# Performance work log

Hardware: AMD Instinct MI355X
Metric: run time of the kernel (lower is better)

Reference implementation:

```python
import jax, jax.numpy as jnp
import numpy as np

# SLAYER neuron / simulation parameters (from network.yaml)
THETA = 10.0      # spike threshold
TAU_SR = 10.0     # SRM (psp) kernel time constant
TAU_REF = 1.0     # refractory kernel time constant
SCALE_REF = 2.0   # refractory scale (kernel = -scaleRef*theta*alpha(t))
TS = 1.0          # simulation step (ms)
TK = 100          # FIR truncation length for the psp kernel (tauSr=10 -> fully decayed)

B, NIN, NHID, NOUT, T = 32, 2312, 512, 10, 350

# discrete refractory kernel ref[n] = C_REF * n * D_REF**n  (alpha shape)
D_REF = float(np.exp(-TS / TAU_REF))
C_REF = float(-SCALE_REF * THETA * np.e * TS / TAU_REF)


def srm_kernel():
    # eps(t) = (t/tauSr) * exp(1 - t/tauSr), peak value 1 at t = tauSr
    t = jnp.arange(TK, dtype=jnp.float32) * TS
    return (t / TAU_SR) * jnp.exp(1.0 - t / TAU_SR)


def psp(x):
    """Causal FIR filter along time. x: [B, C, T] -> [B, C, T]."""
    b, c, t = x.shape
    k = srm_kernel()[::-1].reshape(1, 1, TK)  # lax.conv correlates, so flip
    xp = jnp.pad(x.reshape(b * c, 1, t), ((0, 0), (0, 0), (TK - 1, 0)))
    y = jax.lax.conv_general_dilated(xp, k, (1,), 'VALID')
    return y.reshape(b, c, t)


def dense(W, x):
    # 1x1 conv over channels, applied at every time step
    return jnp.einsum('oi,bit->bot', W, x)


@jax.custom_vjp
def spike_fn(u):
    return (u >= THETA).astype(u.dtype)

def _spike_fwd(u):
    return spike_fn(u), u

def _spike_bwd(u, g):
    # SLAYER surrogate gradient: rho(u) = scaleRho * exp(-|u - theta| / tauRho)
    return (g * jnp.exp(-jnp.abs(u - THETA) / 1.0),)

spike_fn.defvjp(_spike_fwd, _spike_bwd)


def spike_layer(u_in):
    """Threshold-and-refractory spike dynamics via a 2-state IIR realization of
    the alpha refractory kernel. u_in: [B, C, T] -> spikes [B, C, T]."""
    uT = jnp.moveaxis(u_in, -1, 0)  # [T, B, C]
    zero = jnp.zeros(uT.shape[1:], uT.dtype)

    def step(carry, u_t):
        a, b = carry  # a = conv(spikes, D^n), b = conv(spikes, n*D^n)
        u = u_t + C_REF * b          # membrane = psp drive + refractory
        s = spike_fn(u)
        a_new = D_REF * a + s
        b_new = D_REF * b + D_REF * a
        return (a_new, b_new), s

    _, sT = jax.lax.scan(step, (zero, zero), uT)
    return jnp.moveaxis(sT, 0, -1)


def setup_inputs() -> dict:
    key = jax.random.key(0)
    k1, k2, k3 = jax.random.split(key, 3)
    spikeInput = (jax.random.uniform(k1, (B, NIN, T)) < 0.05).astype(jnp.float32)
    W1 = jax.random.normal(k2, (NHID, NIN), dtype=jnp.float32) * 0.05
    W2 = jax.random.normal(k3, (NOUT, NHID), dtype=jnp.float32) * 0.05
    return {"spikeInput": spikeInput, "W1": W1, "W2": W2}


def reference(spikeInput, W1, W2):
    s1 = spike_layer(dense(W1, psp(spikeInput)))
    s2 = spike_layer(dense(W2, psp(s1)))
    return s2
```

## Files before the change

### kernel.cpp

```cpp
#include <hip/hip_runtime.h>
#include <stdint.h>

#define B_SZ   32
#define NIN    2312
#define NHID   512
#define NOUT   10
#define T_SZ   350
#define NW32   73
#define NW64   8
#define NHALF  256
#define NROW   2313

#define DS_D   0.9048374180359595
#define CS_D   0.2718281828459045
#define D100_D 4.5399929762484854e-05
#define DREF_F 0.36787944117144233f
#define CREF_F -54.36563656918091f

#define NCHUNK 7
#define CLEN   50
#define NPF    10

__global__ __launch_bounds__(384) void k12(const float* __restrict__ x,
                                           const float* __restrict__ W1,
                                           uint32_t* __restrict__ bits1,
                                           float* __restrict__ W1s) {
    __shared__ float lds[32 * T_SZ];
    const int bid = blockIdx.x;
    const int tid = threadIdx.x;
    if (bid < NW32 * B_SZ) {
        const int w = bid % NW32;
        const int b = bid / NW32;
        const int rows = (NIN - (w << 5) < 32) ? (NIN - (w << 5)) : 32;
        const float* base = x + ((size_t)(b * NIN + (w << 5))) * T_SZ;
        const int nf4 = (rows * T_SZ) >> 2;
        for (int f = tid; f < nf4; f += 384)
            ((float4*)lds)[f] = ((const float4*)base)[f];
        __syncthreads();
        if (tid < T_SZ) {
            uint32_t bits = 0;
            for (int j = 0; j < rows; ++j)
                bits |= (lds[j * T_SZ + tid] > 0.5f) ? (1u << j) : 0u;
            bits1[(size_t)(b * T_SZ + tid) * NW32 + w] = bits;
        }
    } else if (bid < NW32 * B_SZ + NW32 * 16) {
        float (*tile)[33] = (float (*)[33])lds;
        const int bb = bid - NW32 * B_SZ;
        const int i0 = (bb % NW32) * 32, o0 = (bb / NW32) * 32;
        const int tx = tid & 31, ty = tid >> 5;
#pragma unroll
        for (int r = 0; r < 3; ++r) {
            int row = ty + 12 * r;
            if (row < 32) {
                int o = o0 + row, i = i0 + tx;
                if (i < NIN) tile[row][tx] = W1[(size_t)o * NIN + i];
            }
        }
        __syncthreads();
#pragma unroll
        for (int r = 0; r < 3; ++r) {
            int row = ty + 12 * r;
            if (row < 32) {
                int i = i0 + row, o = o0 + tx;
                if (i < NIN)
                    W1s[((size_t)(o >> 8) * NROW + i) * NHALF + (o & 255)] = tile[tx][row];
            }
        }
    } else {
        if (tid < NHALF) {
            W1s[((size_t)0 * NROW + NIN) * NHALF + tid] = 0.0f;
            W1s[((size_t)1 * NROW + NIN) * NHALF + tid] = 0.0f;
        }
    }
}

__global__ __launch_bounds__(256) void k3_dense1(const uint32_t* __restrict__ bits1,
                                                 const float* __restrict__ W1s,
                                                 float* __restrict__ z1ct) {
    __shared__ uint32_t words[128];
    __shared__ uint16_t pfx[80];
    __shared__ uint16_t idxbuf[NIN + 16];
    __shared__ float red[3][NHALF];
    __shared__ float fin[NHALF];

    const int id = blockIdx.x;
    const int h = (id >> 2) & 1;
    const int bt = ((id >> 3) << 2) | (id & 3);
    const int tid = threadIdx.x;
    const int wv = tid >> 6, lane = tid & 63;

    if (tid < 128) words[tid] = (tid < NW32) ? bits1[(size_t)bt * NW32 + tid] : 0u;
    __syncthreads();

    if (wv == 0) {
        uint32_t w0 = words[lane];
        uint32_t w1 = words[lane + 64];
        int p0 = __popc(w0), p1 = __popc(w1);
        int s0 = p0, s1 = p1;
#pragma unroll
        for (int off = 1; off < 64; off <<= 1) {
            int u0 = __shfl_up(s0, off);
            int u1 = __shfl_up(s1, off);
            if (lane >= off) { s0 += u0; s1 += u1; }
        }
        int tot0 = __shfl(s0, 63);
        pfx[lane] = (uint16_t)(s0 - p0);
        if (lane < 9) pfx[lane + 64] = (uint16_t)(tot0 + s1 - p1);
        if (lane == 8) pfx[73] = (uint16_t)(tot0 + s1);
    }
    __syncthreads();

    const int ntot = pfx[73];
    const int npad = (ntot + 15) & ~15;
    if (tid < NW32) {
        uint32_t m = words[tid];
        int p = pfx[tid];
        while (m) {
            int j = __builtin_ctz(m);
            m &= m - 1;
            idxbuf[p++] = (uint16_t)((tid << 5) + j);
        }
    }
    if (tid >= 240) {
        int k = tid - 240;
        if (ntot + k < npad) idxbuf[ntot + k] = (uint16_t)NIN;
    }
    __syncthreads();

    const float* Wh = W1s + (size_t)h * NROW * NHALF;
    float4 acc = make_float4(0.f, 0.f, 0.f, 0.f);
    for (int r = wv; r < npad; r += 16) {
        int i0 = idxbuf[r], i1 = idxbuf[r + 4], i2 = idxbuf[r + 8], i3 = idxbuf[r + 12];
        float4 v0 = ((const float4*)(Wh + (size_t)i0 * NHALF))[lane];
        float4 v1 = ((const float4*)(Wh + (size_t)i1 * NHALF))[lane];
        float4 v2 = ((const float4*)(Wh + (size_t)i2 * NHALF))[lane];
        float4 v3 = ((const float4*)(Wh + (size_t)i3 * NHALF))[lane];
        acc.x += v0.x; acc.y += v0.y; acc.z += v0.z; acc.w += v0.w;
        acc.x += v1.x; acc.y += v1.y; acc.z += v1.z; acc.w += v1.w;
        acc.x += v2.x; acc.y += v2.y; acc.z += v2.z; acc.w += v2.w;
        acc.x += v3.x; acc.y += v3.y; acc.z += v3.z; acc.w += v3.w;
    }
    if (wv > 0) ((float4*)red[wv - 1])[lane] = acc;
    __syncthreads();
    if (wv == 0) {
        float4 a1 = ((float4*)red[0])[lane];
        float4 a2 = ((float4*)red[1])[lane];
        float4 a3 = ((float4*)red[2])[lane];
        acc.x = ((acc.x + a1.x) + a2.x) + a3.x;
        acc.y = ((acc.y + a1.y) + a2.y) + a3.y;
        acc.z = ((acc.z + a1.z) + a2.z) + a3.z;
        acc.w = ((acc.w + a1.w) + a2.w) + a3.w;
        ((float4*)fin)[lane] = acc;
    }
    __syncthreads();
    const int och = (h << 8) + tid;
    const int oc = och >> 6, l6 = och & 63;
    const int b = bt / T_SZ, t = bt - b * T_SZ;
    z1ct[((size_t)(b * NW64 + oc) * T_SZ + t) * 64 + l6] = fin[tid];
}

__global__ __launch_bounds__(512) void k45(const float* __restrict__ z1ct,
                                           const float* __restrict__ W2,
                                           float* __restrict__ z2ct) {
    __shared__ float W2s[NHID * NOUT];
    __shared__ uint64_t sw[CLEN][NW64];
    const int tid = threadIdx.x;
    const int wv = tid >> 6, lane = tid & 63;
    const int b = blockIdx.x / NCHUNK;
    const int ck = blockIdx.x % NCHUNK;
    const int tstart = ck * CLEN;
    const int tend = tstart + CLEN;
    const int t0 = (tstart >= 100) ? tstart - 100 : 0;

    for (int k = tid; k < NHID * NOUT; k += 512) {
        int c = k / NOUT, o = k - c * NOUT;
        W2s[k] = W2[(size_t)o * NHID + c];
    }

    const float* base = z1ct + (size_t)(b * NW64 + wv) * T_SZ * 64 + lane;
    double A = 0.0, Bs = 0.0, A2 = 0.0, Bs2 = 0.0;
    float ra = 0.0f, rb = 0.0f;
    const double TAIL = D100_D * CS_D;
    float xb[NPF], xdb[NPF];
#pragma unroll
    for (int i = 0; i < NPF; ++i) {
        int t = t0 + i;
        xb[i] = base[(size_t)t * 64];
        int td = t - 100;
        xdb[i] = (td >= 0) ? base[(size_t)td * 64] : 0.0f;
    }
    for (int tb = t0; tb < tend; tb += NPF) {
#pragma unroll
        for (int i = 0; i < NPF; ++i) {
            const int t = tb + i;
            float x = xb[i], xd = xdb[i];
            const int tn = t + NPF;
            xb[i] = (tn < T_SZ) ? base[(size_t)tn * 64] : 0.0f;
            const int td = tn - 100;
            xdb[i] = (td >= 0) ? base[(size_t)td * 64] : 0.0f;
            Bs = DS_D * Bs + DS_D * A;
            A = DS_D * A + (double)x;
            Bs2 = DS_D * Bs2 + DS_D * A2;
            A2 = DS_D * A2 + (double)xd;
            double y = CS_D * Bs - TAIL * (Bs2 + 100.0 * A2);
            float u = (float)y + CREF_F * rb;
            float s = (u >= 10.0f) ? 1.0f : 0.0f;
            float ran = DREF_F * ra + s;
            float rbn = DREF_F * rb + DREF_F * ra;
            ra = ran; rb = rbn;
            uint64_t mball = __ballot(s != 0.0f);
            if (t >= tstart && lane == 0) sw[t - tstart][wv] = mball;
        }
    }
    __syncthreads();

    if (tid < CLEN * NOUT) {
        const int tr = tid / NOUT;
        const int o = tid - tr * NOUT;
        const int t = tstart + tr;
        float acc = 0.f;
#pragma unroll
        for (int w2 = 0; w2 < NW64; ++w2) {
            uint64_t m = sw[tr][w2];
            while (m) {
                int j = __builtin_ctzll(m);
                m &= m - 1;
                acc += W2s[((w2 << 6) + j) * NOUT + o];
            }
        }
        const int bo = b * NOUT + o;
        z2ct[((size_t)(bo >> 6) * T_SZ + t) * 64 + (bo & 63)] = acc;
    }
}

__global__ __launch_bounds__(64) void k6_fir_scan2(const float* __restrict__ z2ct,
                                                   float* __restrict__ out) {
    const int lane = threadIdx.x;
    const int g = blockIdx.x / NCHUNK;
    const int ck = blockIdx.x % NCHUNK;
    const int tstart = ck * CLEN;
    const int tend = tstart + CLEN;
    const int t0 = (tstart >= 100) ? tstart - 100 : 0;
    const int bo = (g << 6) + lane;
    const float* base = z2ct + (size_t)g * T_SZ * 64 + lane;
    float* op = out + (size_t)bo * T_SZ;
    double A = 0.0, Bs = 0.0, A2 = 0.0, Bs2 = 0.0;
    float ra = 0.0f, rb = 0.0f;
    const double TAIL = D100_D * CS_D;
    float xb[NPF], xdb[NPF];
#pragma unroll
    for (int i = 0; i < NPF; ++i) {
        int t = t0 + i;
        xb[i] = base[(size_t)t * 64];
        int td = t - 100;
        xdb[i] = (td >= 0) ? base[(size_t)td * 64] : 0.0f;
    }
    for (int tb = t0; tb < tend; tb += NPF) {
#pragma unroll
        for (int i = 0; i < NPF; ++i) {
            const int t = tb + i;
            float x = xb[i], xd = xdb[i];
            const int tn = t + NPF;
            xb[i] = (tn < T_SZ) ? base[(size_t)tn * 64] : 0.0f;
            const int td = tn - 100;
            xdb[i] = (td >= 0) ? base[(size_t)td * 64] : 0.0f;
            Bs = DS_D * Bs + DS_D * A;
            A = DS_D * A + (double)x;
            Bs2 = DS_D * Bs2 + DS_D * A2;
            A2 = DS_D * A2 + (double)xd;
            double y = CS_D * Bs - TAIL * (Bs2 + 100.0 * A2);
            float u = (float)y + CREF_F * rb;
            float s = (u >= 10.0f) ? 1.0f : 0.0f;
            float ran = DREF_F * ra + s;
            float rbn = DREF_F * rb + DREF_F * ra;
            ra = ran; rb = rbn;
            if (t >= tstart) op[t] = s;
        }
    }
}

extern "C" void kernel_launch(void* const* d_in, const int* in_sizes, int n_in,
                              void* d_out, int out_size, void* d_ws, size_t ws_size,
                              hipStream_t stream) {
    const float* spikeInput = (const float*)d_in[0];
    const float* W1 = (const float*)d_in[1];
    const float* W2 = (const float*)d_in[2];
    float* out = (float*)d_out;

    char* ws = (char*)d_ws;
    float* W1s = (float*)(ws + 0);
    uint32_t* bits1 = (uint32_t*)(ws + 4737024);
    float* z1ct = (float*)(ws + 8007424);
    float* z2ct = (float*)(ws + 4737024);

    k12<<<NW32 * B_SZ + NW32 * 16 + 1, 384, 0, stream>>>(spikeInput, W1, bits1, W1s);
    k3_dense1<<<B_SZ * T_SZ * 2, 256, 0, stream>>>(bits1, W1s, z1ct);
    k45<<<B_SZ * NCHUNK, 512, 0, stream>>>(z1ct, W2, z2ct);
    k6_fir_scan2<<<5 * NCHUNK, 64, 0, stream>>>(z2ct, out);
}
```

Measured before the change: 315.8 us.

## Initialize PSP IIR state directly via 4-way strided decomposition instead of long burn-in

In the second-layer kernel, chunks other than the first no longer replay up to 100 steps of the serial IIR recurrence before their window. Each chunk now seeds the A/Bs state (and the delayed-tail A2/Bs2 state) with four interleaved sub-recurrences using D^4, combined in closed form. The burn-in before the window is cut to 40 steps. This shortens the sequential dependency chain per chunk, at the cost of extra loads and double-precision math up front and a possible change in the spike dynamics' warm-up behaviour.

```diff
diff --git a/kernel.cpp b/kernel.cpp
--- a/kernel.cpp
+++ b/kernel.cpp
@@ -12,6 +12,9 @@
 #define NROW   2313
 
 #define DS_D   0.9048374180359595
+#define DS2_D  0.8187307530779818
+#define DS3_D  0.7408182206817179
+#define DS4_D  0.6703200460356393
 #define CS_D   0.2718281828459045
 #define D100_D 4.5399929762484854e-05
 #define DREF_F 0.36787944117144233f
@@ -19,6 +22,7 @@
 
 #define NCHUNK 7
 #define CLEN   50
+#define BURN   40
 #define NPF    10
 
 __global__ __launch_bounds__(384) void k12(const float* __restrict__ x,
@@ -170,7 +174,7 @@
     const int ck = blockIdx.x % NCHUNK;
     const int tstart = ck * CLEN;
     const int tend = tstart + CLEN;
-    const int t0 = (tstart >= 100) ? tstart - 100 : 0;
+    const int t0 = (ck == 0) ? 0 : tstart - BURN;
 
     for (int k = tid; k < NHID * NOUT; k += 512) {
         int c = k / NOUT, o = k - c * NOUT;
@@ -181,6 +185,43 @@
     double A = 0.0, Bs = 0.0, A2 = 0.0, Bs2 = 0.0;
     float ra = 0.0f, rb = 0.0f;
     const double TAIL = D100_D * CS_D;
+
+    if (ck != 0) {
+        const int hi1 = t0 - 1;
+        const int hi2 = t0 - 101;
+        double F0=0,F1=0,F2=0,F3=0, G0=0,G1=0,G2=0,G3=0;
+        double P0=0,P1=0,P2=0,P3=0, Q0=0,Q1=0,Q2=0,Q3=0;
+#pragma unroll
+        for (int q = 0; q < 25; ++q) {
+            const int ta3 = hi1 - 99 + 4 * q;
+            float x3 = 0.f, x2 = 0.f, x1 = 0.f, x0 = 0.f;
+            if (ta3     >= 0) x3 = base[(size_t)(ta3    ) * 64];
+            if (ta3 + 1 >= 0) x2 = base[(size_t)(ta3 + 1) * 64];
+            if (ta3 + 2 >= 0) x1 = base[(size_t)(ta3 + 2) * 64];
+            if (ta3 + 3 >= 0) x0 = base[(size_t)(ta3 + 3) * 64];
+            G3 = DS4_D * G3 + DS4_D * F3; F3 = DS4_D * F3 + (double)x3;
+            G2 = DS4_D * G2 + DS4_D * F2; F2 = DS4_D * F2 + (double)x2;
+            G1 = DS4_D * G1 + DS4_D * F1; F1 = DS4_D * F1 + (double)x1;
+            G0 = DS4_D * G0 + DS4_D * F0; F0 = DS4_D * F0 + (double)x0;
+            const int tb3 = hi2 - 99 + 4 * q;
+            float y3 = 0.f, y2 = 0.f, y1 = 0.f, y0 = 0.f;
+            if (tb3     >= 0) y3 = base[(size_t)(tb3    ) * 64];
+            if (tb3 + 1 >= 0) y2 = base[(size_t)(tb3 + 1) * 64];
+            if (tb3 + 2 >= 0) y1 = base[(size_t)(tb3 + 2) * 64];
+            if (tb3 + 3 >= 0) y0 = base[(size_t)(tb3 + 3) * 64];
+            Q3 = DS4_D * Q3 + DS4_D * P3; P3 = DS4_D * P3 + (double)y3;
+            Q2 = DS4_D * Q2 + DS4_D * P2; P2 = DS4_D * P2 + (double)y2;
+            Q1 = DS4_D * Q1 + DS4_D * P1; P1 = DS4_D * P1 + (double)y1;
+            Q0 = DS4_D * Q0 + DS4_D * P0; P0 = DS4_D * P0 + (double)y0;
+        }
+        A   = F0 + DS_D * F1 + DS2_D * F2 + DS3_D * F3;
+        Bs  = 4.0 * G0 + DS_D * (F1 + 4.0 * G1)
+            + DS2_D * (2.0 * F2 + 4.0 * G2) + DS3_D * (3.0 * F3 + 4.0 * G3);
+        A2  = P0 + DS_D * P1 + DS2_D * P2 + DS3_D * P3;
+        Bs2 = 4.0 * Q0 + DS_D * (P1 + 4.0 * Q1)
+            + DS2_D * (2.0 * P2 + 4.0 * Q2) + DS3_D * (3.0 * P3 + 4.0 * Q3);
+    }
+
     float xb[NPF], xdb[NPF];
 #pragma unroll
     for (int i = 0; i < NPF; ++i) {
```

After: 376.7 us. +19.3%, slower.

## Split fused scan+dense2 kernel into full-length scan and separate dense2

Applied to the files above, without the earlier changes.

The fused k45 kernel, which recomputed a 100-step warmup window of the first-layer FIR/refractory scan for each of seven time chunks, is split in two. A new scan kernel runs each 64-channel group once over the whole time axis and writes spike ballots to workspace, and a separate dense2 kernel reads those ballots per chunk. This removes the redundant warmup recomputation, but the scan becomes one long serial pass per wave across only 256 single-wave blocks. It also adds an extra launch and a global round trip for the ballots.

```diff
diff --git a/kernel.cpp b/kernel.cpp
--- a/kernel.cpp
+++ b/kernel.cpp
@@ -20,6 +20,7 @@
 #define NCHUNK 7
 #define CLEN   50
 #define NPF    10
+#define SNPF   14
 
 __global__ __launch_bounds__(384) void k12(const float* __restrict__ x,
                                            const float* __restrict__ W1,
@@ -159,42 +160,29 @@
     z1ct[((size_t)(b * NW64 + oc) * T_SZ + t) * 64 + l6] = fin[tid];
 }
 
-__global__ __launch_bounds__(512) void k45(const float* __restrict__ z1ct,
-                                           const float* __restrict__ W2,
-                                           float* __restrict__ z2ct) {
-    __shared__ float W2s[NHID * NOUT];
-    __shared__ uint64_t sw[CLEN][NW64];
-    const int tid = threadIdx.x;
-    const int wv = tid >> 6, lane = tid & 63;
-    const int b = blockIdx.x / NCHUNK;
-    const int ck = blockIdx.x % NCHUNK;
-    const int tstart = ck * CLEN;
-    const int tend = tstart + CLEN;
-    const int t0 = (tstart >= 100) ? tstart - 100 : 0;
-
-    for (int k = tid; k < NHID * NOUT; k += 512) {
-        int c = k / NOUT, o = k - c * NOUT;
-        W2s[k] = W2[(size_t)o * NHID + c];
-    }
-
-    const float* base = z1ct + (size_t)(b * NW64 + wv) * T_SZ * 64 + lane;
+__global__ __launch_bounds__(64) void k4_scan1(const float* __restrict__ z1ct,
+                                               uint64_t* __restrict__ ballots) {
+    const int lane = threadIdx.x;
+    const int bg = blockIdx.x;
+    const float* base = z1ct + (size_t)bg * T_SZ * 64 + lane;
+    const int b = bg >> 3, g = bg & 7;
+    uint64_t* bout = ballots + (size_t)b * T_SZ * NW64 + g;
+
     double A = 0.0, Bs = 0.0, A2 = 0.0, Bs2 = 0.0;
     float ra = 0.0f, rb = 0.0f;
     const double TAIL = D100_D * CS_D;
-    float xb[NPF], xdb[NPF];
-#pragma unroll
-    for (int i = 0; i < NPF; ++i) {
-        int t = t0 + i;
-        xb[i] = base[(size_t)t * 64];
-        int td = t - 100;
-        xdb[i] = (td >= 0) ? base[(size_t)td * 64] : 0.0f;
-    }
-    for (int tb = t0; tb < tend; tb += NPF) {
-#pragma unroll
-        for (int i = 0; i < NPF; ++i) {
+    float xb[SNPF], xdb[SNPF];
+#pragma unroll
+    for (int i = 0; i < SNPF; ++i) {
+        xb[i] = base[(size_t)i * 64];
+        xdb[i] = 0.0f;
+    }
+    for (int tb = 0; tb < T_SZ; tb += SNPF) {
+#pragma unroll
+        for (int i = 0; i < SNPF; ++i) {
             const int t = tb + i;
             float x = xb[i], xd = xdb[i];
-            const int tn = t + NPF;
+            const int tn = t + SNPF;
             xb[i] = (tn < T_SZ) ? base[(size_t)tn * 64] : 0.0f;
             const int td = tn - 100;
             xdb[i] = (td >= 0) ? base[(size_t)td * 64] : 0.0f;
@@ -209,8 +197,28 @@
             float rbn = DREF_F * rb + DREF_F * ra;
             ra = ran; rb = rbn;
             uint64_t mball = __ballot(s != 0.0f);
-            if (t >= tstart && lane == 0) sw[t - tstart][wv] = mball;
-        }
+            if (lane == 0) bout[(size_t)t * NW64] = mball;
+        }
+    }
+}
+
+__global__ __launch_bounds__(512) void k5_dense2(const uint64_t* __restrict__ ballots,
+                                                 const float* __restrict__ W2,
+                                                 float* __restrict__ z2ct) {
+    __shared__ float W2s[NHID * NOUT];
+    __shared__ uint64_t sw[CLEN][NW64];
+    const int tid = threadIdx.x;
+    const int b = blockIdx.x / NCHUNK;
+    const int ck = blockIdx.x % NCHUNK;
+    const int tstart = ck * CLEN;
+
+    for (int k = tid; k < NHID * NOUT; k += 512) {
+        int c = k / NOUT, o = k - c * NOUT;
+        W2s[k] = W2[(size_t)o * NHID + c];
+    }
+    if (tid < CLEN * NW64) {
+        const int tr = tid >> 3, g = tid & 7;
+        sw[tr][g] = ballots[((size_t)(b * T_SZ + tstart + tr)) * NW64 + g];
     }
     __syncthreads();
 
@@ -292,9 +300,11 @@
     uint32_t* bits1 = (uint32_t*)(ws + 4737024);
     float* z1ct = (float*)(ws + 8007424);
     float* z2ct = (float*)(ws + 4737024);
+    uint64_t* ballots = (uint64_t*)(ws + 5185024);
 
     k12<<<NW32 * B_SZ + NW32 * 16 + 1, 384, 0, stream>>>(spikeInput, W1, bits1, W1s);
     k3_dense1<<<B_SZ * T_SZ * 2, 256, 0, stream>>>(bits1, W1s, z1ct);
-    k45<<<B_SZ * NCHUNK, 512, 0, stream>>>(z1ct, W2, z2ct);
+    k4_scan1<<<B_SZ * NW64, 64, 0, stream>>>(z1ct, ballots);
+    k5_dense2<<<B_SZ * NCHUNK, 512, 0, stream>>>(ballots, W2, z2ct);
     k6_fir_scan2<<<5 * NCHUNK, 64, 0, stream>>>(z2ct, out);
 }
```

After: 332.5 us. +5.3%, slower.
